# Kernel optimization log

Measured on AMD Instinct MI355X. Metric: run time of the kernel, lower is better.

The kernel has to match this reference:

```python
import jax, jax.numpy as jnp
import numpy as np

LR = 0.001
TAU = 1000.0


def setup_inputs() -> dict:
    key = jax.random.key(0)
    k1, k2 = jax.random.split(key)
    B, IN, OUT = 8192, 4096, 4096
    x = jax.random.normal(k1, (B, IN), dtype=jnp.float32)
    weight = jax.random.normal(k2, (OUT, IN), dtype=jnp.float32) * 0.1
    threshold = jnp.zeros((OUT,), dtype=jnp.float32)
    return {"x": x, "weight": weight, "threshold": threshold}


def reference(x, weight, threshold):
    # output = x @ W.T  -> (B, out)
    output = jnp.matmul(x, weight.T)

    # BCM sliding-threshold EMA (torch uses output.detach())
    activity = jnp.mean(jax.lax.stop_gradient(output), axis=0)  # (out,)
    new_threshold = threshold + (activity ** 2 - threshold) / TAU

    # Hebbian update: torch builds (B, out, in) outer products then means over B;
    # equivalent efficient form: post.T @ pre / B (single GEMM).
    post = jax.lax.stop_gradient(jnp.maximum(output - new_threshold, 0.0))  # (B, out)
    B = x.shape[0]
    delta_w = (LR / B) * jnp.einsum('bo,bi->oi', post, x)
    new_weight = weight + delta_w

    # Original returns (output, threshold-after-update); we also expose the
    # updated weight (the in-place .data side effect) for verification.
    return output, new_threshold, new_weight
```

## Files before the change

kernel.cpp:

```cpp
#include <hip/hip_runtime.h>
#include <hip/hip_bf16.h>


typedef __attribute__((ext_vector_type(8))) short   bf16x8;
typedef __attribute__((ext_vector_type(4))) float   f32x4;

#define ASG __attribute__((address_space(1)))
#define ASL __attribute__((address_space(3)))

__device__ __forceinline__ void gload16(const void* g, void* l) {
    __builtin_amdgcn_global_load_lds((const ASG void*)g, (ASL void*)l, 16, 0, 0);
}

__device__ __forceinline__ unsigned short f2bf(float x) {
    union { float f; unsigned u; } v; v.f = x;
    unsigned r = v.u;
    r += 0x7fffu + ((r >> 16) & 1u);
    return (unsigned short)(r >> 16);
}
__device__ __forceinline__ float bf2f(unsigned short u) {
    union { unsigned u; float f; } v; v.u = ((unsigned)u) << 16;
    return v.f;
}

__global__ __launch_bounds__(256) void k_cvt_split(const float* __restrict__ src,
                                                   unsigned short* __restrict__ hi,
                                                   unsigned short* __restrict__ lo,
                                                   int n4) {
    int i = blockIdx.x * blockDim.x + threadIdx.x;
    int stride = gridDim.x * blockDim.x;
    for (; i < n4; i += stride) {
        float4 v = reinterpret_cast<const float4*>(src)[i];
        ushort4 h, l;
        h.x = f2bf(v.x); l.x = f2bf(v.x - bf2f(h.x));
        h.y = f2bf(v.y); l.y = f2bf(v.y - bf2f(h.y));
        h.z = f2bf(v.z); l.z = f2bf(v.z - bf2f(h.z));
        h.w = f2bf(v.w); l.w = f2bf(v.w - bf2f(h.w));
        reinterpret_cast<ushort4*>(hi)[i] = h;
        reinterpret_cast<ushort4*>(lo)[i] = l;
    }
}

__global__ __launch_bounds__(256) void k_gemm1(const unsigned short* __restrict__ Ah,
                                               const unsigned short* __restrict__ Al,
                                               const unsigned short* __restrict__ Bh,
                                               const unsigned short* __restrict__ Bl,
                                               float* __restrict__ C) {
    const int K = 4096, N = 4096;
    __shared__ unsigned short lAh[128 * 64], lAl[128 * 64], lBh[128 * 64], lBl[128 * 64];

    const int t    = threadIdx.x;
    const int lane = t & 63, wid = t >> 6;
    const int ln15 = lane & 15, l16 = lane >> 4;
    const int wm   = wid >> 1, wn = wid & 1;
    const int bm   = blockIdx.y, bn = blockIdx.x;

    const int srow   = lane >> 3;
    const int schunk = (lane & 7) ^ (srow & 7);
    const size_t aBase = (size_t)(bm * 128 + wid * 8 + srow) * K + schunk * 8;
    const size_t bBase = (size_t)(bn * 128 + wid * 8 + srow) * K + schunk * 8;

    f32x4 acc[4][4];
#pragma unroll
    for (int i = 0; i < 4; ++i)
#pragma unroll
        for (int j = 0; j < 4; ++j) acc[i][j] = (f32x4){0.f, 0.f, 0.f, 0.f};

    for (int k0 = 0; k0 < K; k0 += 64) {
        __syncthreads();
#pragma unroll
        for (int i = 0; i < 4; ++i) {
            const int g = i * 4 + wid;
            const size_t ro = (size_t)i * 32 * K;
            const int lo_ = g * 512 + lane * 8;
            gload16(Ah + aBase + ro + k0, &lAh[lo_]);
            gload16(Al + aBase + ro + k0, &lAl[lo_]);
            gload16(Bh + bBase + ro + k0, &lBh[lo_]);
            gload16(Bl + bBase + ro + k0, &lBl[lo_]);
        }
        __syncthreads();

#pragma unroll
        for (int kk = 0; kk < 2; ++kk) {
            bf16x8 ah[4], al[4], bh[4], bl[4];
#pragma unroll
            for (int mi = 0; mi < 4; ++mi) {
                const int r   = wm * 64 + mi * 16 + ln15;
                const int idx = r * 64 + (((l16 + kk * 4) ^ (r & 7)) * 8);
                ah[mi] = *(const bf16x8*)&lAh[idx];
                al[mi] = *(const bf16x8*)&lAl[idx];
            }
#pragma unroll
            for (int ni = 0; ni < 4; ++ni) {
                const int r   = wn * 64 + ni * 16 + ln15;
                const int idx = r * 64 + (((l16 + kk * 4) ^ (r & 7)) * 8);
                bh[ni] = *(const bf16x8*)&lBh[idx];
                bl[ni] = *(const bf16x8*)&lBl[idx];
            }
#pragma unroll
            for (int mi = 0; mi < 4; ++mi)
#pragma unroll
                for (int ni = 0; ni < 4; ++ni) {
                    acc[mi][ni] = __builtin_amdgcn_mfma_f32_16x16x32_bf16(ah[mi], bh[ni], acc[mi][ni], 0, 0, 0);
                    acc[mi][ni] = __builtin_amdgcn_mfma_f32_16x16x32_bf16(ah[mi], bl[ni], acc[mi][ni], 0, 0, 0);
                    acc[mi][ni] = __builtin_amdgcn_mfma_f32_16x16x32_bf16(al[mi], bh[ni], acc[mi][ni], 0, 0, 0);
                }
        }
    }

    const int row0 = bm * 128 + wm * 64;
    const int col0 = bn * 128 + wn * 64;
#pragma unroll
    for (int mi = 0; mi < 4; ++mi)
#pragma unroll
        for (int ni = 0; ni < 4; ++ni)
#pragma unroll
            for (int j = 0; j < 4; ++j) {
                const int row = row0 + mi * 16 + l16 * 4 + j;
                const int col = col0 + ni * 16 + ln15;
                C[(size_t)row * N + col] = acc[mi][ni][j];
            }
}

__global__ __launch_bounds__(256) void k_gemm2(const unsigned short* __restrict__ A,
                                               const unsigned short* __restrict__ Bx,
                                               const float* __restrict__ Wf,
                                               float* __restrict__ Wout, float scale) {
    const int K = 8192, N = 4096;
    __shared__ unsigned short lA[128 * 64], lB[128 * 64];

    const int t    = threadIdx.x;
    const int lane = t & 63, wid = t >> 6;
    const int ln15 = lane & 15, l16 = lane >> 4;
    const int wm   = wid >> 1, wn = wid & 1;
    const int bm   = blockIdx.y, bn = blockIdx.x;

    const int srow   = lane >> 3;
    const int schunk = (lane & 7) ^ (srow & 7);
    const size_t aBase = (size_t)(bm * 128 + wid * 8 + srow) * K + schunk * 8;
    const size_t bBase = (size_t)(bn * 128 + wid * 8 + srow) * K + schunk * 8;

    f32x4 acc[4][4];
#pragma unroll
    for (int i = 0; i < 4; ++i)
#pragma unroll
        for (int j = 0; j < 4; ++j) acc[i][j] = (f32x4){0.f, 0.f, 0.f, 0.f};

    for (int k0 = 0; k0 < K; k0 += 64) {
        __syncthreads();
#pragma unroll
        for (int i = 0; i < 4; ++i) {
            const int g = i * 4 + wid;
            const size_t ro = (size_t)i * 32 * K;
            const int lo_ = g * 512 + lane * 8;
            gload16(A + aBase + ro + k0, &lA[lo_]);
            gload16(Bx + bBase + ro + k0, &lB[lo_]);
        }
        __syncthreads();

#pragma unroll
        for (int kk = 0; kk < 2; ++kk) {
            bf16x8 a[4], b[4];
#pragma unroll
            for (int mi = 0; mi < 4; ++mi) {
                const int r   = wm * 64 + mi * 16 + ln15;
                const int idx = r * 64 + (((l16 + kk * 4) ^ (r & 7)) * 8);
                a[mi] = *(const bf16x8*)&lA[idx];
            }
#pragma unroll
            for (int ni = 0; ni < 4; ++ni) {
                const int r   = wn * 64 + ni * 16 + ln15;
                const int idx = r * 64 + (((l16 + kk * 4) ^ (r & 7)) * 8);
                b[ni] = *(const bf16x8*)&lB[idx];
            }
#pragma unroll
            for (int mi = 0; mi < 4; ++mi)
#pragma unroll
                for (int ni = 0; ni < 4; ++ni)
                    acc[mi][ni] = __builtin_amdgcn_mfma_f32_16x16x32_bf16(a[mi], b[ni], acc[mi][ni], 0, 0, 0);
        }
    }

    const int row0 = bm * 128 + wm * 64;
    const int col0 = bn * 128 + wn * 64;
#pragma unroll
    for (int mi = 0; mi < 4; ++mi)
#pragma unroll
        for (int ni = 0; ni < 4; ++ni)
#pragma unroll
            for (int j = 0; j < 4; ++j) {
                const int row = row0 + mi * 16 + l16 * 4 + j;
                const int col = col0 + ni * 16 + ln15;
                const size_t idx = (size_t)row * N + col;
                Wout[idx] = Wf[idx] + scale * acc[mi][ni][j];
            }
}

__global__ __launch_bounds__(256) void k_colsum(const float* __restrict__ out,
                                                float* __restrict__ acc) {
    const int col = blockIdx.x * 256 + threadIdx.x;
    const int r0  = blockIdx.y * 128;
    float s = 0.f;
#pragma unroll 4
    for (int r = 0; r < 128; ++r) s += out[(size_t)(r0 + r) * 4096 + col];
    atomicAdd(&acc[col], s);
}

__global__ __launch_bounds__(256) void k_thr(const float* __restrict__ acc,
                                             const float* __restrict__ thr_in,
                                             float* __restrict__ thr_out) {
    const int o = blockIdx.x * 256 + threadIdx.x;
    const float act = acc[o] * (1.0f / 8192.0f);
    const float t0  = thr_in[o];
    thr_out[o] = t0 + (act * act - t0) / 1000.0f;
}

__global__ __launch_bounds__(256) void k_postT(const float* __restrict__ out,
                                               const float* __restrict__ thr,
                                               unsigned short* __restrict__ postT) {
    __shared__ unsigned short tile[64][65];
    __shared__ float sthr[64];
    const int b0 = blockIdx.y * 64, o0 = blockIdx.x * 64;
    if (threadIdx.x < 64) sthr[threadIdx.x] = thr[o0 + threadIdx.x];
    __syncthreads();
#pragma unroll
    for (int it = 0; it < 16; ++it) {
        int idx = it * 256 + threadIdx.x;
        int r = idx >> 6, c = idx & 63;
        float v = out[(size_t)(b0 + r) * 4096 + o0 + c] - sthr[c];
        tile[r][c] = f2bf(v > 0.f ? v : 0.f);
    }
    __syncthreads();
#pragma unroll
    for (int it = 0; it < 16; ++it) {
        int idx = it * 256 + threadIdx.x;
        int r = idx >> 6, c = idx & 63;
        postT[(size_t)(o0 + r) * 8192 + b0 + c] = tile[c][r];
    }
}

__global__ __launch_bounds__(256) void k_xT(const float* __restrict__ x,
                                            unsigned short* __restrict__ xT) {
    __shared__ unsigned short tile[64][65];
    const int b0 = blockIdx.y * 64, i0 = blockIdx.x * 64;
#pragma unroll
    for (int it = 0; it < 16; ++it) {
        int idx = it * 256 + threadIdx.x;
        int r = idx >> 6, c = idx & 63;
        tile[r][c] = f2bf(x[(size_t)(b0 + r) * 4096 + i0 + c]);
    }
    __syncthreads();
#pragma unroll
    for (int it = 0; it < 16; ++it) {
        int idx = it * 256 + threadIdx.x;
        int r = idx >> 6, c = idx & 63;
        xT[(size_t)(i0 + r) * 8192 + b0 + c] = tile[c][r];
    }
}

extern "C" void kernel_launch(void* const* d_in, const int* in_sizes, int n_in,
                              void* d_out, int out_size, void* d_ws, size_t ws_size,
                              hipStream_t stream) {
    const float* x   = (const float*)d_in[0];
    const float* w   = (const float*)d_in[1];
    const float* thr = (const float*)d_in[2];
    const int B = 8192, IN = 4096, OUT = 4096;

    float* out_y   = (float*)d_out;
    float* out_thr = out_y + (size_t)B * OUT;
    float* out_w   = out_thr + OUT;

    char* ws = (char*)d_ws;
    float* acc_act       = (float*)ws;
    unsigned short* x_hi = (unsigned short*)(ws + 65536);
    unsigned short* x_lo = x_hi + (size_t)B * IN;
    unsigned short* w_hi = x_lo + (size_t)B * IN;
    unsigned short* w_lo = w_hi + (size_t)OUT * IN;
    unsigned short* postT = x_lo;
    unsigned short* xT    = w_hi;
    (void)w_lo; (void)ws_size;

    hipMemsetAsync(acc_act, 0, OUT * sizeof(float), stream);

    k_cvt_split<<<2048, 256, 0, stream>>>(x, x_hi, x_lo, B * IN / 4);
    k_cvt_split<<<2048, 256, 0, stream>>>(w, w_hi, w_lo, OUT * IN / 4);

    k_gemm1<<<dim3(OUT / 128, B / 128), 256, 0, stream>>>(x_hi, x_lo, w_hi, w_lo, out_y);

    k_colsum<<<dim3(OUT / 256, B / 128), 256, 0, stream>>>(out_y, acc_act);
    k_thr<<<OUT / 256, 256, 0, stream>>>(acc_act, thr, out_thr);

    k_postT<<<dim3(OUT / 64, B / 64), 256, 0, stream>>>(out_y, out_thr, postT);
    k_xT<<<dim3(IN / 64, B / 64), 256, 0, stream>>>(x, xT);

    k_gemm2<<<dim3(IN / 128, OUT / 128), 256, 0, stream>>>(postT, xT, w, out_w,
                                                           (float)(0.001 / 8192.0));
}
```

Baseline: 1.438 ms.

## Restructure both GEMMs with 256x128 tiles, triple-buffered LDS, and fused column sums

Both GEMM kernels move to 512-thread blocks with 256x128 output tiles and a three-stage LDS ring, prefetched two k-steps ahead using async global-to-LDS loads and vmcnt waits instead of full syncthreads. Blocks are remapped across groups of eight for cache locality, and MFMA sections run at raised wave priority. gemm1 also fuses the column-sum reduction into its epilogue with shuffles and atomics, which removes the separate colsum pass over the output. This trades more registers and LDS per block for fewer barriers, more data reuse and one fewer launch.

```diff
diff --git a/kernel.cpp b/kernel.cpp
--- a/kernel.cpp
+++ b/kernel.cpp
@@ -41,169 +41,203 @@
     }
 }
 
-__global__ __launch_bounds__(256) void k_gemm1(const unsigned short* __restrict__ Ah,
-                                               const unsigned short* __restrict__ Al,
-                                               const unsigned short* __restrict__ Bh,
-                                               const unsigned short* __restrict__ Bl,
-                                               float* __restrict__ C) {
-    const int K = 4096, N = 4096;
-    __shared__ unsigned short lAh[128 * 64], lAl[128 * 64], lBh[128 * 64], lBl[128 * 64];
-
-    const int t    = threadIdx.x;
-    const int lane = t & 63, wid = t >> 6;
-    const int ln15 = lane & 15, l16 = lane >> 4;
-    const int wm   = wid >> 1, wn = wid & 1;
-    const int bm   = blockIdx.y, bn = blockIdx.x;
-
-    const int srow   = lane >> 3;
-    const int schunk = (lane & 7) ^ (srow & 7);
-    const size_t aBase = (size_t)(bm * 128 + wid * 8 + srow) * K + schunk * 8;
-    const size_t bBase = (size_t)(bn * 128 + wid * 8 + srow) * K + schunk * 8;
-
-    f32x4 acc[4][4];
-#pragma unroll
-    for (int i = 0; i < 4; ++i)
-#pragma unroll
-        for (int j = 0; j < 4; ++j) acc[i][j] = (f32x4){0.f, 0.f, 0.f, 0.f};
-
-    for (int k0 = 0; k0 < K; k0 += 64) {
-        __syncthreads();
-#pragma unroll
-        for (int i = 0; i < 4; ++i) {
-            const int g = i * 4 + wid;
-            const size_t ro = (size_t)i * 32 * K;
-            const int lo_ = g * 512 + lane * 8;
-            gload16(Ah + aBase + ro + k0, &lAh[lo_]);
-            gload16(Al + aBase + ro + k0, &lAl[lo_]);
-            gload16(Bh + bBase + ro + k0, &lBh[lo_]);
-            gload16(Bl + bBase + ro + k0, &lBl[lo_]);
+__global__ __launch_bounds__(512, 2) void k_gemm1(const unsigned short* __restrict__ Ah,
+                                                  const unsigned short* __restrict__ Al,
+                                                  const unsigned short* __restrict__ Bh,
+                                                  const unsigned short* __restrict__ Bl,
+                                                  float* __restrict__ C,
+                                                  float* __restrict__ acc_act) {
+    __shared__ unsigned short sm[3 * 24576];
+    const int t = threadIdx.x, lane = t & 63, ln15 = lane & 15, l16 = lane >> 4;
+    const int wid = t >> 6, wm = wid >> 2, wn = wid & 3;
+    const int nwg = gridDim.x, bid = blockIdx.x;
+    const int wg  = (bid & 7) * (nwg >> 3) + (bid >> 3);
+    const int bm = wg >> 5, bn = wg & 31;
+    const int arow0 = bm * 256, brow0 = bn * 128;
+
+    const unsigned short* gsrc[6];
+    int ldso[6];
+#pragma unroll
+    for (int j = 0; j < 6; ++j) {
+        const int c = j * 512 + t;
+        if (c < 1024)      { int cc = c;        int row = cc >> 2, chk = (cc & 3) ^ (row & 3); gsrc[j] = Ah + (size_t)(arow0 + row) * 4096 + chk * 8; ldso[j] = cc * 8; }
+        else if (c < 2048) { int cc = c - 1024; int row = cc >> 2, chk = (cc & 3) ^ (row & 3); gsrc[j] = Al + (size_t)(arow0 + row) * 4096 + chk * 8; ldso[j] = 8192 + cc * 8; }
+        else if (c < 2560) { int cc = c - 2048; int row = cc >> 2, chk = (cc & 3) ^ (row & 3); gsrc[j] = Bh + (size_t)(brow0 + row) * 4096 + chk * 8; ldso[j] = 16384 + cc * 8; }
+        else               { int cc = c - 2560; int row = cc >> 2, chk = (cc & 3) ^ (row & 3); gsrc[j] = Bl + (size_t)(brow0 + row) * 4096 + chk * 8; ldso[j] = 20480 + cc * 8; }
+    }
+
+    int aoh[8], aol[8], boh[2], bol[2];
+#pragma unroll
+    for (int mi = 0; mi < 8; ++mi) {
+        const int r = wm * 128 + mi * 16 + ln15;
+        const int sw = (l16 ^ (r & 3)) * 8;
+        aoh[mi] = r * 32 + sw; aol[mi] = 8192 + r * 32 + sw;
+    }
+#pragma unroll
+    for (int ni = 0; ni < 2; ++ni) {
+        const int r = wn * 32 + ni * 16 + ln15;
+        const int sw = (l16 ^ (r & 3)) * 8;
+        boh[ni] = 16384 + r * 32 + sw; bol[ni] = 20480 + r * 32 + sw;
+    }
+
+    f32x4 acc[8][2];
+#pragma unroll
+    for (int mi = 0; mi < 8; ++mi)
+#pragma unroll
+        for (int ni = 0; ni < 2; ++ni) acc[mi][ni] = (f32x4){0.f, 0.f, 0.f, 0.f};
+
+#pragma unroll
+    for (int j = 0; j < 6; ++j) gload16(gsrc[j], sm + ldso[j]);
+#pragma unroll
+    for (int j = 0; j < 6; ++j) gload16(gsrc[j] + 32, sm + 24576 + ldso[j]);
+
+    int scur = 0, snxt = 2;
+    for (int kt = 0; kt < 128; ++kt) {
+        asm volatile("s_waitcnt vmcnt(6)" ::: "memory");
+        __builtin_amdgcn_s_barrier();
+        asm volatile("" ::: "memory");
+        const unsigned short* rb = sm + scur * 24576;
+        bf16x8 vah[8], val[8], vbh[2], vbl[2];
+#pragma unroll
+        for (int mi = 0; mi < 8; ++mi) { vah[mi] = *(const bf16x8*)(rb + aoh[mi]); val[mi] = *(const bf16x8*)(rb + aol[mi]); }
+#pragma unroll
+        for (int ni = 0; ni < 2; ++ni) { vbh[ni] = *(const bf16x8*)(rb + boh[ni]); vbl[ni] = *(const bf16x8*)(rb + bol[ni]); }
+        {
+            const size_t ko = (size_t)((kt + 2 < 128) ? kt + 2 : 127) * 32;
+            unsigned short* sb = sm + snxt * 24576;
+#pragma unroll
+            for (int j = 0; j < 6; ++j) gload16(gsrc[j] + ko, sb + ldso[j]);
         }
-        __syncthreads();
-
-#pragma unroll
-        for (int kk = 0; kk < 2; ++kk) {
-            bf16x8 ah[4], al[4], bh[4], bl[4];
-#pragma unroll
-            for (int mi = 0; mi < 4; ++mi) {
-                const int r   = wm * 64 + mi * 16 + ln15;
-                const int idx = r * 64 + (((l16 + kk * 4) ^ (r & 7)) * 8);
-                ah[mi] = *(const bf16x8*)&lAh[idx];
-                al[mi] = *(const bf16x8*)&lAl[idx];
+        __builtin_amdgcn_s_setprio(1);
+#pragma unroll
+        for (int mi = 0; mi < 8; ++mi)
+#pragma unroll
+            for (int ni = 0; ni < 2; ++ni) {
+                acc[mi][ni] = __builtin_amdgcn_mfma_f32_16x16x32_bf16(vah[mi], vbh[ni], acc[mi][ni], 0, 0, 0);
+                acc[mi][ni] = __builtin_amdgcn_mfma_f32_16x16x32_bf16(vah[mi], vbl[ni], acc[mi][ni], 0, 0, 0);
+                acc[mi][ni] = __builtin_amdgcn_mfma_f32_16x16x32_bf16(val[mi], vbh[ni], acc[mi][ni], 0, 0, 0);
             }
-#pragma unroll
-            for (int ni = 0; ni < 4; ++ni) {
-                const int r   = wn * 64 + ni * 16 + ln15;
-                const int idx = r * 64 + (((l16 + kk * 4) ^ (r & 7)) * 8);
-                bh[ni] = *(const bf16x8*)&lBh[idx];
-                bl[ni] = *(const bf16x8*)&lBl[idx];
-            }
-#pragma unroll
-            for (int mi = 0; mi < 4; ++mi)
-#pragma unroll
-                for (int ni = 0; ni < 4; ++ni) {
-                    acc[mi][ni] = __builtin_amdgcn_mfma_f32_16x16x32_bf16(ah[mi], bh[ni], acc[mi][ni], 0, 0, 0);
-                    acc[mi][ni] = __builtin_amdgcn_mfma_f32_16x16x32_bf16(ah[mi], bl[ni], acc[mi][ni], 0, 0, 0);
-                    acc[mi][ni] = __builtin_amdgcn_mfma_f32_16x16x32_bf16(al[mi], bh[ni], acc[mi][ni], 0, 0, 0);
-                }
+        __builtin_amdgcn_s_setprio(0);
+        scur = (scur == 2) ? 0 : scur + 1;
+        snxt = (snxt == 2) ? 0 : snxt + 1;
+    }
+    asm volatile("s_waitcnt vmcnt(0)" ::: "memory");
+
+    const int row0 = bm * 256 + wm * 128, col0 = bn * 128 + wn * 32;
+    float cs0 = 0.f, cs1 = 0.f;
+#pragma unroll
+    for (int mi = 0; mi < 8; ++mi)
+#pragma unroll
+        for (int j = 0; j < 4; ++j) {
+            const int row = row0 + mi * 16 + l16 * 4 + j;
+            C[(size_t)row * 4096 + col0 + ln15]      = acc[mi][0][j];
+            C[(size_t)row * 4096 + col0 + 16 + ln15] = acc[mi][1][j];
+            cs0 += acc[mi][0][j]; cs1 += acc[mi][1][j];
         }
-    }
-
-    const int row0 = bm * 128 + wm * 64;
-    const int col0 = bn * 128 + wn * 64;
-#pragma unroll
-    for (int mi = 0; mi < 4; ++mi)
-#pragma unroll
-        for (int ni = 0; ni < 4; ++ni)
-#pragma unroll
-            for (int j = 0; j < 4; ++j) {
-                const int row = row0 + mi * 16 + l16 * 4 + j;
-                const int col = col0 + ni * 16 + ln15;
-                C[(size_t)row * N + col] = acc[mi][ni][j];
-            }
-}
-
-__global__ __launch_bounds__(256) void k_gemm2(const unsigned short* __restrict__ A,
-                                               const unsigned short* __restrict__ Bx,
-                                               const float* __restrict__ Wf,
-                                               float* __restrict__ Wout, float scale) {
-    const int K = 8192, N = 4096;
-    __shared__ unsigned short lA[128 * 64], lB[128 * 64];
-
-    const int t    = threadIdx.x;
-    const int lane = t & 63, wid = t >> 6;
-    const int ln15 = lane & 15, l16 = lane >> 4;
-    const int wm   = wid >> 1, wn = wid & 1;
-    const int bm   = blockIdx.y, bn = blockIdx.x;
-
-    const int srow   = lane >> 3;
-    const int schunk = (lane & 7) ^ (srow & 7);
-    const size_t aBase = (size_t)(bm * 128 + wid * 8 + srow) * K + schunk * 8;
-    const size_t bBase = (size_t)(bn * 128 + wid * 8 + srow) * K + schunk * 8;
-
-    f32x4 acc[4][4];
-#pragma unroll
-    for (int i = 0; i < 4; ++i)
-#pragma unroll
-        for (int j = 0; j < 4; ++j) acc[i][j] = (f32x4){0.f, 0.f, 0.f, 0.f};
-
-    for (int k0 = 0; k0 < K; k0 += 64) {
-        __syncthreads();
-#pragma unroll
-        for (int i = 0; i < 4; ++i) {
-            const int g = i * 4 + wid;
-            const size_t ro = (size_t)i * 32 * K;
-            const int lo_ = g * 512 + lane * 8;
-            gload16(A + aBase + ro + k0, &lA[lo_]);
-            gload16(Bx + bBase + ro + k0, &lB[lo_]);
+    cs0 += __shfl_xor(cs0, 16, 64); cs0 += __shfl_xor(cs0, 32, 64);
+    cs1 += __shfl_xor(cs1, 16, 64); cs1 += __shfl_xor(cs1, 32, 64);
+    if (l16 == 0) {
+        atomicAdd(&acc_act[col0 + ln15], cs0);
+        atomicAdd(&acc_act[col0 + 16 + ln15], cs1);
+    }
+}
+
+__global__ __launch_bounds__(512, 2) void k_gemm2(const unsigned short* __restrict__ A,
+                                                  const unsigned short* __restrict__ Bx,
+                                                  const float* __restrict__ Wf,
+                                                  float* __restrict__ Wout, float scale) {
+    __shared__ unsigned short sm[3 * 24576];
+    const int t = threadIdx.x, lane = t & 63, ln15 = lane & 15, l16 = lane >> 4;
+    const int wid = t >> 6, wm = wid >> 2, wn = wid & 3;
+    const int nwg = gridDim.x, bid = blockIdx.x;
+    const int wg  = (bid & 7) * (nwg >> 3) + (bid >> 3);
+    const int bm = wg >> 5, bn = wg & 31;
+    const int arow0 = bm * 256, brow0 = bn * 128;
+
+    const unsigned short* gsrc[6];
+    int ldso[6];
+#pragma unroll
+    for (int j = 0; j < 6; ++j) {
+        const int c = j * 512 + t;
+        if (c < 2048) { int row = c >> 3, chk = (c & 7) ^ (row & 7); gsrc[j] = A + (size_t)(arow0 + row) * 8192 + chk * 8; ldso[j] = c * 8; }
+        else { int cc = c - 2048; int row = cc >> 3, chk = (cc & 7) ^ (row & 7); gsrc[j] = Bx + (size_t)(brow0 + row) * 8192 + chk * 8; ldso[j] = 16384 + cc * 8; }
+    }
+
+    int ao0[8], ao1[8], bo0[2], bo1[2];
+#pragma unroll
+    for (int mi = 0; mi < 8; ++mi) {
+        const int r = wm * 128 + mi * 16 + ln15;
+        ao0[mi] = r * 64 + ((l16 ^ (r & 7)) * 8);
+        ao1[mi] = r * 64 + (((4 + l16) ^ (r & 7)) * 8);
+    }
+#pragma unroll
+    for (int ni = 0; ni < 2; ++ni) {
+        const int r = wn * 32 + ni * 16 + ln15;
+        bo0[ni] = 16384 + r * 64 + ((l16 ^ (r & 7)) * 8);
+        bo1[ni] = 16384 + r * 64 + (((4 + l16) ^ (r & 7)) * 8);
+    }
+
+    f32x4 acc[8][2];
+#pragma unroll
+    for (int mi = 0; mi < 8; ++mi)
+#pragma unroll
+        for (int ni = 0; ni < 2; ++ni) acc[mi][ni] = (f32x4){0.f, 0.f, 0.f, 0.f};
+
+#pragma unroll
+    for (int j = 0; j < 6; ++j) gload16(gsrc[j], sm + ldso[j]);
+#pragma unroll
+    for (int j = 0; j < 6; ++j) gload16(gsrc[j] + 64, sm + 24576 + ldso[j]);
+
+    int scur = 0, snxt = 2;
+    for (int kt = 0; kt < 128; ++kt) {
+        asm volatile("s_waitcnt vmcnt(6)" ::: "memory");
+        __builtin_amdgcn_s_barrier();
+        asm volatile("" ::: "memory");
+        const unsigned short* rb = sm + scur * 24576;
+        bf16x8 va[8], vb[2];
+#pragma unroll
+        for (int mi = 0; mi < 8; ++mi) va[mi] = *(const bf16x8*)(rb + ao0[mi]);
+#pragma unroll
+        for (int ni = 0; ni < 2; ++ni) vb[ni] = *(const bf16x8*)(rb + bo0[ni]);
+        { const size_t ko = (size_t)((kt + 2 < 128) ? kt + 2 : 127) * 64;
+          unsigned short* sb = sm + snxt * 24576;
+#pragma unroll
+          for (int j = 0; j < 6; ++j) gload16(gsrc[j] + ko, sb + ldso[j]);
         }
-        __syncthreads();
-
-#pragma unroll
-        for (int kk = 0; kk < 2; ++kk) {
-            bf16x8 a[4], b[4];
-#pragma unroll
-            for (int mi = 0; mi < 4; ++mi) {
-                const int r   = wm * 64 + mi * 16 + ln15;
-                const int idx = r * 64 + (((l16 + kk * 4) ^ (r & 7)) * 8);
-                a[mi] = *(const bf16x8*)&lA[idx];
-            }
-#pragma unroll
-            for (int ni = 0; ni < 4; ++ni) {
-                const int r   = wn * 64 + ni * 16 + ln15;
-                const int idx = r * 64 + (((l16 + kk * 4) ^ (r & 7)) * 8);
-                b[ni] = *(const bf16x8*)&lB[idx];
-            }
-#pragma unroll
-            for (int mi = 0; mi < 4; ++mi)
-#pragma unroll
-                for (int ni = 0; ni < 4; ++ni)
-                    acc[mi][ni] = __builtin_amdgcn_mfma_f32_16x16x32_bf16(a[mi], b[ni], acc[mi][ni], 0, 0, 0);
+        __builtin_amdgcn_s_setprio(1);
+#pragma unroll
+        for (int mi = 0; mi < 8; ++mi)
+#pragma unroll
+            for (int ni = 0; ni < 2; ++ni)
+                acc[mi][ni] = __builtin_amdgcn_mfma_f32_16x16x32_bf16(va[mi], vb[ni], acc[mi][ni], 0, 0, 0);
+        __builtin_amdgcn_s_setprio(0);
+#pragma unroll
+        for (int mi = 0; mi < 8; ++mi) va[mi] = *(const bf16x8*)(rb + ao1[mi]);
+#pragma unroll
+        for (int ni = 0; ni < 2; ++ni) vb[ni] = *(const bf16x8*)(rb + bo1[ni]);
+        __builtin_amdgcn_s_setprio(1);
+#pragma unroll
+        for (int mi = 0; mi < 8; ++mi)
+#pragma unroll
+            for (int ni = 0; ni < 2; ++ni)
+                acc[mi][ni] = __builtin_amdgcn_mfma_f32_16x16x32_bf16(va[mi], vb[ni], acc[mi][ni], 0, 0, 0);
+        __builtin_amdgcn_s_setprio(0);
+        scur = (scur == 2) ? 0 : scur + 1;
+        snxt = (snxt == 2) ? 0 : snxt + 1;
+    }
+    asm volatile("s_waitcnt vmcnt(0)" ::: "memory");
+
+    const int row0 = bm * 256 + wm * 128, col0 = bn * 128 + wn * 32;
+#pragma unroll
+    for (int mi = 0; mi < 8; ++mi)
+#pragma unroll
+        for (int j = 0; j < 4; ++j) {
+            const int row = row0 + mi * 16 + l16 * 4 + j;
+            const size_t i0 = (size_t)row * 4096 + col0 + ln15;
+            const size_t i1 = i0 + 16;
+            Wout[i0] = Wf[i0] + scale * acc[mi][0][j];
+            Wout[i1] = Wf[i1] + scale * acc[mi][1][j];
         }
-    }
-
-    const int row0 = bm * 128 + wm * 64;
-    const int col0 = bn * 128 + wn * 64;
-#pragma unroll
-    for (int mi = 0; mi < 4; ++mi)
-#pragma unroll
-        for (int ni = 0; ni < 4; ++ni)
-#pragma unroll
-            for (int j = 0; j < 4; ++j) {
-                const int row = row0 + mi * 16 + l16 * 4 + j;
-                const int col = col0 + ni * 16 + ln15;
-                const size_t idx = (size_t)row * N + col;
-                Wout[idx] = Wf[idx] + scale * acc[mi][ni][j];
-            }
-}
-
-__global__ __launch_bounds__(256) void k_colsum(const float* __restrict__ out,
-                                                float* __restrict__ acc) {
-    const int col = blockIdx.x * 256 + threadIdx.x;
-    const int r0  = blockIdx.y * 128;
-    float s = 0.f;
-#pragma unroll 4
-    for (int r = 0; r < 128; ++r) s += out[(size_t)(r0 + r) * 4096 + col];
-    atomicAdd(&acc[col], s);
 }
 
 __global__ __launch_bounds__(256) void k_thr(const float* __restrict__ acc,
@@ -285,14 +319,12 @@
     k_cvt_split<<<2048, 256, 0, stream>>>(x, x_hi, x_lo, B * IN / 4);
     k_cvt_split<<<2048, 256, 0, stream>>>(w, w_hi, w_lo, OUT * IN / 4);
 
-    k_gemm1<<<dim3(OUT / 128, B / 128), 256, 0, stream>>>(x_hi, x_lo, w_hi, w_lo, out_y);
-
-    k_colsum<<<dim3(OUT / 256, B / 128), 256, 0, stream>>>(out_y, acc_act);
+    k_gemm1<<<1024, 512, 0, stream>>>(x_hi, x_lo, w_hi, w_lo, out_y, acc_act);
+
     k_thr<<<OUT / 256, 256, 0, stream>>>(acc_act, thr, out_thr);
 
     k_postT<<<dim3(OUT / 64, B / 64), 256, 0, stream>>>(out_y, out_thr, postT);
     k_xT<<<dim3(IN / 64, B / 64), 256, 0, stream>>>(x, xT);
 
-    k_gemm2<<<dim3(IN / 128, OUT / 128), 256, 0, stream>>>(postT, xT, w, out_w,
-                                                           (float)(0.001 / 8192.0));
-}
+    k_gemm2<<<512, 512, 0, stream>>>(postT, xT, w, out_w, (float)(0.001 / 8192.0));
+}
```

Result: faster. 1.387 ms (-3.5%).
